# Kernel tuning notes

Measured on AMD Instinct MI355X. Metric: run time of the kernel, lower is better.

Reference implementation:

```python
import jax, jax.numpy as jnp
import numpy as np

N_NODES = 100000
N_EDGES = 500000
N_REL = 6
IN_DIM = 64
HID = 128
HEADS = 4
C = HID // HEADS  # 32 per-head channels
N_GRAPHS = 1024
EPS = 1e-16


def setup_inputs() -> dict:
    key = jax.random.key(0)
    ks = jax.random.split(key, 20)
    x = jax.random.normal(ks[0], (N_NODES, IN_DIM), dtype=jnp.float32)
    edge_index = jax.random.randint(ks[1], (N_REL, 2, N_EDGES), 0, N_NODES, dtype=jnp.int64)
    batch = jnp.sort(jax.random.randint(ks[2], (N_NODES,), 0, N_GRAPHS, dtype=jnp.int64))
    s = 0.02
    return {
        "x": x, "edge_index": edge_index, "batch": batch,
        # layer1 GAT params (stacked over 6 relations)
        "W1": jax.random.normal(ks[3], (N_REL, IN_DIM, HID), dtype=jnp.float32) * s,
        "as1": jax.random.normal(ks[4], (N_REL, HEADS, C), dtype=jnp.float32) * s,
        "ad1": jax.random.normal(ks[5], (N_REL, HEADS, C), dtype=jnp.float32) * s,
        "b1": jnp.zeros((N_REL, HID), dtype=jnp.float32),
        # layer2 GAT params
        "W2": jax.random.normal(ks[6], (N_REL, HID, HID), dtype=jnp.float32) * s,
        "as2": jax.random.normal(ks[7], (N_REL, HEADS, C), dtype=jnp.float32) * s,
        "ad2": jax.random.normal(ks[8], (N_REL, HEADS, C), dtype=jnp.float32) * s,
        "b2": jnp.zeros((N_REL, HID), dtype=jnp.float32),
        # layernorms
        "g1": jnp.ones((HID,), dtype=jnp.float32), "be1": jnp.zeros((HID,), dtype=jnp.float32),
        "g2": jnp.ones((HID,), dtype=jnp.float32), "be2": jnp.zeros((HID,), dtype=jnp.float32),
        # attention pooling query + output proj
        "q": jax.random.normal(ks[9], (HID,), dtype=jnp.float32) * s,
        "Wp": jax.random.normal(ks[10], (HID, HID), dtype=jnp.float32) * s,
        "bp": jnp.zeros((HID,), dtype=jnp.float32),
    }


def _gat_hetero_layer(x, edge_index, W, a_src, a_dst, b):
    # HeteroConv(aggr='sum') over R GATConv relations, add_self_loops=False, eval (no dropout)
    N = x.shape[0]
    out = jnp.zeros((N, HEADS * C), dtype=x.dtype)
    for r in range(N_REL):
        h = (x @ W[r]).reshape(N, HEADS, C)          # [N,H,C]
        al_s = (h * a_src[r]).sum(-1)                # [N,H]
        al_d = (h * a_dst[r]).sum(-1)                # [N,H]
        src, dst = edge_index[r, 0], edge_index[r, 1]
        e = jax.nn.leaky_relu(al_s[src] + al_d[dst], 0.2)   # [E,H]
        m = jax.ops.segment_max(e, dst, num_segments=N)
        ex = jnp.exp(e - m[dst])
        den = jax.ops.segment_sum(ex, dst, num_segments=N)
        alpha = ex / (den[dst] + EPS)                # segment softmax over incoming edges
        msg = h[src] * alpha[:, :, None]             # [E,H,C]
        agg = jax.ops.segment_sum(msg, dst, num_segments=N).reshape(N, HEADS * C)
        out = out + agg + b[r]
    return out


def _layernorm(x, g, b):
    mu = x.mean(-1, keepdims=True)
    v = ((x - mu) ** 2).mean(-1, keepdims=True)
    return (x - mu) * jax.lax.rsqrt(v + 1e-5) * g + b


def _softsign(x):
    return x / (1.0 + jnp.abs(x))


def reference(x, edge_index, batch, W1, as1, ad1, b1, W2, as2, ad2, b2,
              g1, be1, g2, be2, q, Wp, bp):
    h = _gat_hetero_layer(x, edge_index, W1, as1, ad1, b1)
    h = _layernorm(_softsign(h), g1, be1)
    h = _gat_hetero_layer(h, edge_index, W2, as2, ad2, b2)
    h = _layernorm(_softsign(h), g2, be2)
    # attention pooling: segment softmax over batch, then weighted scatter-sum
    scores = (h * q).sum(-1)                                   # [N]
    m = jax.ops.segment_max(scores, batch, num_segments=N_GRAPHS)
    ex = jnp.exp(scores - m[batch])
    den = jax.ops.segment_sum(ex, batch, num_segments=N_GRAPHS)
    w = ex / (den[batch] + EPS)
    pooled = jax.ops.segment_sum(h * w[:, None], batch, num_segments=N_GRAPHS)  # [G,HID]
    return pooled @ Wp + bp
```

## Files before the change

kernel.cpp:

```cpp
#include <hip/hip_runtime.h>
#include <hip/hip_bf16.h>
#include <hip/hip_fp16.h>

#define N_NODES_C 100000
#define N_EDGES_C 500000
#define N_REL_C 6
#define IN_DIM_C 64
#define HID_C 128
#define HEADS_C 4
#define CPH_C 32
#define N_GRAPHS_C 1024
#define NBLK_SCAN 391
#define SH_PAD 8

typedef _Float16 f16x8 __attribute__((ext_vector_type(8)));
typedef float f32x4 __attribute__((ext_vector_type(4)));

__global__ __launch_bounds__(256) void hist_rank_convert_kernel(
    const int* __restrict__ ei, int* __restrict__ cnt, int* __restrict__ rank,
    const float* __restrict__ x, __half* __restrict__ xh,
    const float* __restrict__ W1, const float* __restrict__ W2,
    __half* __restrict__ Wt1, __half* __restrict__ Wt2) {
    int i = blockIdx.x * 256 + threadIdx.x;
    if (i < N_NODES_C * IN_DIM_C / 4) {
        float4 v = ((const float4*)x)[i];
        union { __half h[4]; uint2 u; } u;
        u.h[0] = __float2half(v.x); u.h[1] = __float2half(v.y);
        u.h[2] = __float2half(v.z); u.h[3] = __float2half(v.w);
        ((uint2*)xh)[i] = u.u;
    }
    if (i < N_REL_C * IN_DIM_C * HID_C) {
        int r = i / (IN_DIM_C * HID_C);
        int rem = i - r * (IN_DIM_C * HID_C);
        int k = rem / HID_C, n = rem - k * HID_C;
        Wt1[(size_t)r * HID_C * IN_DIM_C + n * IN_DIM_C + k] = __float2half(W1[i]);
    }
    if (i < N_REL_C * HID_C * HID_C) {
        int r = i / (HID_C * HID_C);
        int rem = i - r * (HID_C * HID_C);
        int k = rem / HID_C, n = rem - k * HID_C;
        Wt2[(size_t)r * HID_C * HID_C + n * HID_C + k] = __float2half(W2[i]);
    }
    if (i < N_REL_C * N_EDGES_C) {
        int r = i / N_EDGES_C;
        int e = i - r * N_EDGES_C;
        int dst = ei[(size_t)r * 2 * N_EDGES_C + N_EDGES_C + e];
        rank[i] = atomicAdd(&cnt[r * N_NODES_C + dst], 1);
    }
}

__global__ __launch_bounds__(256) void scan1_kernel(const int* __restrict__ cnt,
                                                    int* __restrict__ rowptr,
                                                    int* __restrict__ blocksums) {
    int r = blockIdx.y, b = blockIdx.x, t = threadIdx.x;
    int idx = b * 256 + t;
    int v = (idx < N_NODES_C) ? cnt[r * N_NODES_C + idx] : 0;
    int orig = v;
    int lane = t & 63, w = t >> 6;
#pragma unroll
    for (int off = 1; off < 64; off <<= 1) {
        int n = __shfl_up(v, off);
        if (lane >= off) v += n;
    }
    __shared__ int wt[4];
    if (lane == 63) wt[w] = v;
    __syncthreads();
    int add = 0;
    for (int i = 0; i < w; i++) add += wt[i];
    v += add;
    if (idx < N_NODES_C) rowptr[(size_t)r * (N_NODES_C + 1) + idx] = v - orig;
    if (t == 255) blocksums[r * NBLK_SCAN + b] = v;
}

__global__ __launch_bounds__(512) void scan2_kernel(int* __restrict__ blocksums) {
    int r = blockIdx.x, t = threadIdx.x;
    int v = (t < NBLK_SCAN) ? blocksums[r * NBLK_SCAN + t] : 0;
    int orig = v;
    int lane = t & 63, w = t >> 6;
#pragma unroll
    for (int off = 1; off < 64; off <<= 1) {
        int n = __shfl_up(v, off);
        if (lane >= off) v += n;
    }
    __shared__ int wt[8];
    if (lane == 63) wt[w] = v;
    __syncthreads();
    int add = 0;
    for (int i = 0; i < w; i++) add += wt[i];
    v += add;
    if (t < NBLK_SCAN) blocksums[r * NBLK_SCAN + t] = v - orig;
}

__global__ __launch_bounds__(256) void scatter_kernel(const int* __restrict__ ei,
                                                      const int* __restrict__ rowptrP,
                                                      const int* __restrict__ bsums,
                                                      const int* __restrict__ rank,
                                                      int* __restrict__ srcids) {
    int i = blockIdx.x * 256 + threadIdx.x;
    if (i >= N_REL_C * N_EDGES_C) return;
    int r = i / N_EDGES_C;
    int e = i - r * N_EDGES_C;
    int src = ei[(size_t)r * 2 * N_EDGES_C + e];
    int dst = ei[(size_t)r * 2 * N_EDGES_C + N_EDGES_C + e];
    int base = rowptrP[(size_t)r * (N_NODES_C + 1) + dst] + bsums[r * NBLK_SCAN + (dst >> 8)];
    srcids[(size_t)r * N_EDGES_C + base + rank[i]] = src;
}

template <int K>
__global__ __launch_bounds__(256) void gemm_mfma_kernel(
    const __half* __restrict__ Xh, const __half* __restrict__ Wtbase,
    __half* __restrict__ Hbase,
    const float* __restrict__ asbase, const float* __restrict__ adbase,
    float* __restrict__ alsbase, float* __restrict__ aldbase) {
    __shared__ _Float16 sh[4][16][HID_C + SH_PAD];
    const int slot = blockIdx.y;
    const __half* Wt = Wtbase + (size_t)slot * HID_C * K;
    __half* H = Hbase + (size_t)slot * N_NODES_C * HID_C;
    const int wave = threadIdx.x >> 6, lane = threadIdx.x & 63;
    const int r0 = blockIdx.x * 64 + wave * 16;
    const int m = lane & 15, quad = lane >> 4;
    int arow = r0 + m;
    if (arow > N_NODES_C - 1) arow = N_NODES_C - 1;
    const __half* ap = Xh + (size_t)arow * K + quad * 8;
    const __half* bp = Wt + (size_t)m * K + quad * 8;

    f32x4 acc[8];
#pragma unroll
    for (int t = 0; t < 8; t++) acc[t] = (f32x4){0.f, 0.f, 0.f, 0.f};

#pragma unroll
    for (int kc = 0; kc < K; kc += 32) {
        f16x8 a = *(const f16x8*)(ap + kc);
#pragma unroll
        for (int t = 0; t < 8; t++) {
            f16x8 b = *(const f16x8*)(bp + (size_t)t * 16 * K + kc);
            acc[t] = __builtin_amdgcn_mfma_f32_16x16x32_f16(a, b, acc[t], 0, 0, 0);
        }
    }

#pragma unroll
    for (int t = 0; t < 8; t++)
#pragma unroll
        for (int i = 0; i < 4; i++)
            sh[wave][quad * 4 + i][t * 16 + m] = (_Float16)acc[t][i];
#pragma unroll
    for (int p = 0; p < 4; p++) {
        int idx = p * 512 + lane * 8;
        int row = idx >> 7;
        int col = idx & 127;
        int R = r0 + row;
        if (R < N_NODES_C)
            *(uint4*)(H + (size_t)R * HID_C + col) = *(const uint4*)&sh[wave][row][col];
    }

    const float* a_s = asbase + slot * HID_C;
    const float* a_d = adbase + slot * HID_C;
    float* als = alsbase + (size_t)slot * N_NODES_C * HEADS_C;
    float* ald = aldbase + (size_t)slot * N_NODES_C * HEADS_C;
    float ps[4][4], pd[4][4];
#pragma unroll
    for (int h = 0; h < 4; h++) {
        float as0 = a_s[h * 32 + m], as1 = a_s[h * 32 + 16 + m];
        float ad0 = a_d[h * 32 + m], ad1 = a_d[h * 32 + 16 + m];
#pragma unroll
        for (int i = 0; i < 4; i++) {
            ps[h][i] = acc[2 * h][i] * as0 + acc[2 * h + 1][i] * as1;
            pd[h][i] = acc[2 * h][i] * ad0 + acc[2 * h + 1][i] * ad1;
        }
    }
#pragma unroll
    for (int off = 1; off < 16; off <<= 1) {
#pragma unroll
        for (int h = 0; h < 4; h++)
#pragma unroll
            for (int i = 0; i < 4; i++) {
                ps[h][i] += __shfl_xor(ps[h][i], off);
                pd[h][i] += __shfl_xor(pd[h][i], off);
            }
    }
#pragma unroll
    for (int h = 0; h < 4; h++) {
        if (m == h) {
#pragma unroll
            for (int i = 0; i < 4; i++) {
                int R = r0 + quad * 4 + i;
                if (R < N_NODES_C) {
                    als[R * HEADS_C + h] = ps[h][i];
                    ald[R * HEADS_C + h] = pd[h][i];
                }
            }
        }
    }
}

__global__ __launch_bounds__(256) void csr_agg_kernel(
    const int* __restrict__ rowptrP, const int* __restrict__ bsums,
    const int* __restrict__ srcids,
    const __half* __restrict__ A, const float* __restrict__ als,
    const float* __restrict__ ald, int rel_start, int rel_cnt,
    const float* __restrict__ bias, int first, int last,
    float* __restrict__ B,
    const float* __restrict__ g, const float* __restrict__ be,
    __half* __restrict__ Cbh) {
    int node = blockIdx.x * 4 + (threadIdx.x >> 6);
    int lane = threadIdx.x & 63;
    int grp = lane >> 4;
    int j16 = lane & 15;
    int head = j16 >> 2;
    int cbase = j16 * 8;

    float acc[8];
    if (first) {
#pragma unroll
        for (int t = 0; t < 8; t++) {
            float s = 0.f;
#pragma unroll
            for (int r = 0; r < N_REL_C; r++) s += bias[r * HID_C + cbase + t];
            acc[t] = s;
        }
    } else {
        float4 b0 = *(const float4*)(B + (size_t)node * HID_C + cbase);
        float4 b1 = *(const float4*)(B + (size_t)node * HID_C + cbase + 4);
        acc[0] = b0.x; acc[1] = b0.y; acc[2] = b0.z; acc[3] = b0.w;
        acc[4] = b1.x; acc[5] = b1.y; acc[6] = b1.z; acc[7] = b1.w;
    }

    for (int j = 0; j < rel_cnt; j++) {
        int r = rel_start + j;
        const int* rp = rowptrP + (size_t)r * (N_NODES_C + 1);
        const int* bs = bsums + r * NBLK_SCAN;
        const int* sp = srcids + (size_t)r * N_EDGES_C;
        const __half* Aj = A + (size_t)j * N_NODES_C * HID_C;
        const float* alj = als + (size_t)j * N_NODES_C * HEADS_C;
        float aldv = ald[(size_t)j * N_NODES_C * HEADS_C + node * HEADS_C + head];
        int s = rp[node] + bs[node >> 8];
        int e = (node == N_NODES_C - 1) ? N_EDGES_C
                                        : rp[node + 1] + bs[(node + 1) >> 8];
        float racc[8];
#pragma unroll
        for (int t = 0; t < 8; t++) racc[t] = 0.f;
        float rden = 0.f;

        union HU { uint4 u; _Float16 h[8]; };
        int i = s + grp;
        int src = (i < e) ? sp[i] : 0;
        HU rw; rw.u = *(const uint4*)(Aj + (size_t)src * HID_C + cbase);
        float lg = alj[src * HEADS_C + head];
        for (; i < e; i += 4) {
            int nsrc = (i + 4 < e) ? sp[i + 4] : 0;
            HU nrw; nrw.u = *(const uint4*)(Aj + (size_t)nsrc * HID_C + cbase);
            float nlg = alj[nsrc * HEADS_C + head];
            float v = lg + aldv;
            v = fmaxf(v, 0.2f * v);
            float ex = __expf(v);
            rden += ex;
#pragma unroll
            for (int t = 0; t < 8; t++)
                racc[t] = fmaf((float)rw.h[t], ex, racc[t]);
            src = nsrc; rw = nrw; lg = nlg;
        }
#pragma unroll
        for (int off = 16; off < 64; off <<= 1) {
            rden += __shfl_xor(rden, off);
#pragma unroll
            for (int t = 0; t < 8; t++) racc[t] += __shfl_xor(racc[t], off);
        }
        float inv = 1.f / (rden + 1e-16f);
#pragma unroll
        for (int t = 0; t < 8; t++) acc[t] = fmaf(racc[t], inv, acc[t]);
    }

    if (!last) {
        if (grp == 0) {
            float4 o0 = make_float4(acc[0], acc[1], acc[2], acc[3]);
            float4 o1 = make_float4(acc[4], acc[5], acc[6], acc[7]);
            *(float4*)(B + (size_t)node * HID_C + cbase) = o0;
            *(float4*)(B + (size_t)node * HID_C + cbase + 4) = o1;
        }
    } else {
        float ss[8];
        float sum = 0.f, sq = 0.f;
#pragma unroll
        for (int t = 0; t < 8; t++) {
            float v = acc[t] / (1.f + fabsf(acc[t]));
            ss[t] = v;
            sum += v;
            sq = fmaf(v, v, sq);
        }
#pragma unroll
        for (int off = 1; off < 16; off <<= 1) {
            sum += __shfl_xor(sum, off);
            sq += __shfl_xor(sq, off);
        }
        float mu = sum * (1.f / 128.f);
        float var = sq * (1.f / 128.f) - mu * mu;
        float inv = rsqrtf(var + 1e-5f);
        if (grp == 0) {
            float4 gv0 = *(const float4*)(g + cbase);
            float4 gv1 = *(const float4*)(g + cbase + 4);
            float4 bv0 = *(const float4*)(be + cbase);
            float4 bv1 = *(const float4*)(be + cbase + 4);
            union { uint4 u; __half2 h2[4]; } ow;
            ow.h2[0] = __float22half2_rn(make_float2(
                (ss[0] - mu) * inv * gv0.x + bv0.x, (ss[1] - mu) * inv * gv0.y + bv0.y));
            ow.h2[1] = __float22half2_rn(make_float2(
                (ss[2] - mu) * inv * gv0.z + bv0.z, (ss[3] - mu) * inv * gv0.w + bv0.w));
            ow.h2[2] = __float22half2_rn(make_float2(
                (ss[4] - mu) * inv * gv1.x + bv1.x, (ss[5] - mu) * inv * gv1.y + bv1.y));
            ow.h2[3] = __float22half2_rn(make_float2(
                (ss[6] - mu) * inv * gv1.z + bv1.z, (ss[7] - mu) * inv * gv1.w + bv1.w));
            *(uint4*)(Cbh + (size_t)node * HID_C + cbase) = ow.u;
        }
    }
}

__device__ __forceinline__ int lower_bound_i(const int* __restrict__ a, int n, int v) {
    int lo = 0, hi = n;
    while (lo < hi) {
        int mid = (lo + hi) >> 1;
        if (a[mid] < v) lo = mid + 1; else hi = mid;
    }
    return lo;
}

__global__ __launch_bounds__(256) void pool_kernel(const __half* __restrict__ H,
                                                   const int* __restrict__ batch,
                                                   const float* __restrict__ q,
                                                   float* __restrict__ pooled) {
    int g = blockIdx.x;
    int t = threadIdx.x;
    int wave = t >> 6, lane = t & 63;
    int start = lower_bound_i(batch, N_NODES_C, g);
    int end = lower_bound_i(batch, N_NODES_C, g + 1);
    float q0 = q[lane * 2], q1 = q[lane * 2 + 1];
    float p0 = 0.f, p1 = 0.f, den = 0.f;
    for (int n = start + wave; n < end; n += 4) {
        float2 hv = __half22float2(*(const __half2*)(H + (size_t)n * HID_C + lane * 2));
        float part = hv.x * q0 + hv.y * q1;
#pragma unroll
        for (int off = 1; off < 64; off <<= 1) part += __shfl_xor(part, off);
        float exs = __expf(part);
        den += exs;
        p0 = fmaf(exs, hv.x, p0);
        p1 = fmaf(exs, hv.y, p1);
    }
    __shared__ float sp[4][HID_C];
    __shared__ float sden[4];
    sp[wave][lane * 2] = p0;
    sp[wave][lane * 2 + 1] = p1;
    if (lane == 0) sden[wave] = den;
    __syncthreads();
    if (wave == 0) {
        float a0 = sp[0][lane * 2] + sp[1][lane * 2] + sp[2][lane * 2] + sp[3][lane * 2];
        float a1 = sp[0][lane * 2 + 1] + sp[1][lane * 2 + 1] + sp[2][lane * 2 + 1] + sp[3][lane * 2 + 1];
        float d = sden[0] + sden[1] + sden[2] + sden[3];
        float w = 1.f / (d + 1e-16f);
        pooled[(size_t)g * HID_C + lane * 2] = a0 * w;
        pooled[(size_t)g * HID_C + lane * 2 + 1] = a1 * w;
    }
}

__global__ __launch_bounds__(128) void proj_kernel(const float* __restrict__ pooled,
                                                   const float* __restrict__ Wp,
                                                   const float* __restrict__ bp,
                                                   float* __restrict__ out) {
    int g = blockIdx.x, c = threadIdx.x;
    __shared__ float pl[HID_C];
    pl[c] = pooled[(size_t)g * HID_C + c];
    __syncthreads();
    float s = bp[c];
    for (int k = 0; k < HID_C; k++) s = fmaf(pl[k], Wp[k * HID_C + c], s);
    out[(size_t)g * HID_C + c] = s;
}

extern "C" void kernel_launch(void* const* d_in, const int* in_sizes, int n_in,
                              void* d_out, int out_size, void* d_ws, size_t ws_size,
                              hipStream_t stream) {
    const float* x   = (const float*)d_in[0];
    const int* ei    = (const int*)d_in[1];
    const int* batch = (const int*)d_in[2];
    const float* W1  = (const float*)d_in[3];
    const float* as1 = (const float*)d_in[4];
    const float* ad1 = (const float*)d_in[5];
    const float* b1  = (const float*)d_in[6];
    const float* W2  = (const float*)d_in[7];
    const float* as2 = (const float*)d_in[8];
    const float* ad2 = (const float*)d_in[9];
    const float* b2  = (const float*)d_in[10];
    const float* g1  = (const float*)d_in[11];
    const float* be1 = (const float*)d_in[12];
    const float* g2  = (const float*)d_in[13];
    const float* be2 = (const float*)d_in[14];
    const float* q   = (const float*)d_in[15];
    const float* Wp  = (const float*)d_in[16];
    const float* bp  = (const float*)d_in[17];
    float* out = (float*)d_out;

    const size_t NH = (size_t)N_NODES_C * HID_C;
    char* w = (char*)d_ws;
    __half* xh    = (__half*)w;   w += (size_t)N_NODES_C * IN_DIM_C * 2;
    __half* Cbh   = (__half*)w;   w += NH * 2;
    __half* Wt1   = (__half*)w;   w += (size_t)N_REL_C * IN_DIM_C * HID_C * 2;
    __half* Wt2   = (__half*)w;   w += (size_t)N_REL_C * HID_C * HID_C * 2;
    float* pooled = (float*)w;    w += (size_t)N_GRAPHS_C * HID_C * 4;
    int* rowptr   = (int*)w;      w += ((size_t)N_REL_C * (N_NODES_C + 1) * 4 + 15) & ~15ull;
    int* srcids   = (int*)w;      w += (size_t)N_REL_C * N_EDGES_C * 4;
    int* cnt      = (int*)w;      w += (size_t)N_REL_C * N_NODES_C * 4;
    int* bsums    = (int*)w;      w += ((size_t)N_REL_C * NBLK_SCAN * 4 + 15) & ~15ull;

    const size_t fixed_bytes = (size_t)(w - (char*)d_ws);
    const size_t slot_bytes = NH * 2 + 2 * (size_t)N_NODES_C * HEADS_C * 4;
    int nA = 1;
    float* B = nullptr;
    {
        size_t rem = (ws_size > fixed_bytes) ? (ws_size - fixed_bytes) : 0;
        size_t k = rem / slot_bytes;
        if (k >= 6) {
            nA = 6;
        } else {
            size_t rem2 = (rem > NH * 4) ? (rem - NH * 4) : 0;
            size_t k2 = rem2 / slot_bytes;
            nA = (int)(k2 < 1 ? 1 : (k2 > 5 ? 5 : k2));
        }
    }
    float* als = (float*)w;
    float* ald = als + (size_t)nA * N_NODES_C * HEADS_C;
    __half* A  = (__half*)(ald + (size_t)nA * N_NODES_C * HEADS_C);
    if (nA < 6) B = (float*)(A + (size_t)nA * NH);
    int* rank = (int*)A;

    hipMemsetAsync(cnt, 0, (size_t)N_REL_C * N_NODES_C * sizeof(int), stream);
    const int ehg = (N_REL_C * N_EDGES_C + 255) / 256;
    hist_rank_convert_kernel<<<ehg, 256, 0, stream>>>(ei, cnt, rank, x, xh, W1, W2, Wt1, Wt2);
    scan1_kernel<<<dim3(NBLK_SCAN, N_REL_C), 256, 0, stream>>>(cnt, rowptr, bsums);
    scan2_kernel<<<N_REL_C, 512, 0, stream>>>(bsums);
    scatter_kernel<<<ehg, 256, 0, stream>>>(ei, rowptr, bsums, rank, srcids);

    const int gemm_grid = (N_NODES_C + 63) / 64;
    const int agg_grid = N_NODES_C / 4;

    for (int gs = 0; gs < N_REL_C; gs += nA) {
        int c2 = (N_REL_C - gs) < nA ? (N_REL_C - gs) : nA;
        gemm_mfma_kernel<IN_DIM_C><<<dim3(gemm_grid, c2), 256, 0, stream>>>(
            xh, Wt1 + (size_t)gs * IN_DIM_C * HID_C, A,
            as1 + gs * HID_C, ad1 + gs * HID_C, als, ald);
        csr_agg_kernel<<<agg_grid, 256, 0, stream>>>(
            rowptr, bsums, srcids, A, als, ald, gs, c2,
            b1, (gs == 0) ? 1 : 0, (gs + c2 == N_REL_C) ? 1 : 0,
            B, g1, be1, Cbh);
    }
    for (int gs = 0; gs < N_REL_C; gs += nA) {
        int c2 = (N_REL_C - gs) < nA ? (N_REL_C - gs) : nA;
        gemm_mfma_kernel<HID_C><<<dim3(gemm_grid, c2), 256, 0, stream>>>(
            Cbh, Wt2 + (size_t)gs * HID_C * HID_C, A,
            as2 + gs * HID_C, ad2 + gs * HID_C, als, ald);
        csr_agg_kernel<<<agg_grid, 256, 0, stream>>>(
            rowptr, bsums, srcids, A, als, ald, gs, c2,
            b2, (gs == 0) ? 1 : 0, (gs + c2 == N_REL_C) ? 1 : 0,
            B, g2, be2, Cbh);
    }

    pool_kernel<<<N_GRAPHS_C, 256, 0, stream>>>(Cbh, batch, q, pooled);
    proj_kernel<<<N_GRAPHS_C, 128, 0, stream>>>(pooled, Wp, bp, out);
}
```

Baseline: 1.043 ms.

## Aggregate raw input features before projection in layer one GAT

Layer one no longer projects every node to 128 channels per relation before aggregating. The attention logits are computed directly from x using folded vectors W1·a. Then the 64-dim fp16 input features are aggregated per head along the CSR edges, and the aggregate is multiplied by W1 with MFMA in a fused kernel that also applies bias, softsign and layernorm. This cuts the 128-wide per-edge gathers down to 64-wide and removes the per-relation projected H buffers. In exchange it does four times the per-head accumulation in registers and rounds the aggregates to fp16 before the MFMA.

```diff
diff --git a/kernel.cpp b/kernel.cpp
--- a/kernel.cpp
+++ b/kernel.cpp
@@ -20,7 +20,9 @@
     const int* __restrict__ ei, int* __restrict__ cnt, int* __restrict__ rank,
     const float* __restrict__ x, __half* __restrict__ xh,
     const float* __restrict__ W1, const float* __restrict__ W2,
-    __half* __restrict__ Wt1, __half* __restrict__ Wt2) {
+    __half* __restrict__ Wt1, __half* __restrict__ Wt2,
+    const float* __restrict__ as1, const float* __restrict__ ad1,
+    float* __restrict__ wsd, float* __restrict__ wdd) {
     int i = blockIdx.x * 256 + threadIdx.x;
     if (i < N_NODES_C * IN_DIM_C / 4) {
         float4 v = ((const float4*)x)[i];
@@ -40,6 +42,19 @@
         int rem = i - r * (HID_C * HID_C);
         int k = rem / HID_C, n = rem - k * HID_C;
         Wt2[(size_t)r * HID_C * HID_C + n * HID_C + k] = __float2half(W2[i]);
+    }
+    if (i < N_REL_C * HEADS_C * IN_DIM_C) {
+        int r = i >> 8, h = (i >> 6) & 3, k = i & 63;
+        const float* wrow = W1 + ((size_t)(r * IN_DIM_C + k)) * HID_C + h * CPH_C;
+        const float* av_s = as1 + (r * HEADS_C + h) * CPH_C;
+        const float* av_d = ad1 + (r * HEADS_C + h) * CPH_C;
+        float ss = 0.f, sd = 0.f;
+#pragma unroll
+        for (int c = 0; c < CPH_C; c++) {
+            ss = fmaf(wrow[c], av_s[c], ss);
+            sd = fmaf(wrow[c], av_d[c], sd);
+        }
+        wsd[i] = ss; wdd[i] = sd;
     }
     if (i < N_REL_C * N_EDGES_C) {
         int r = i / N_EDGES_C;
@@ -104,6 +119,179 @@
     int dst = ei[(size_t)r * 2 * N_EDGES_C + N_EDGES_C + e];
     int base = rowptrP[(size_t)r * (N_NODES_C + 1) + dst] + bsums[r * NBLK_SCAN + (dst >> 8)];
     srcids[(size_t)r * N_EDGES_C + base + rank[i]] = src;
+}
+
+__global__ __launch_bounds__(256) void logit1_kernel(
+    const __half* __restrict__ xh, const float* __restrict__ wsd,
+    const float* __restrict__ wdd, float* __restrict__ als, float* __restrict__ ald) {
+    int wave = threadIdx.x >> 6, lane = threadIdx.x & 63;
+    int node = blockIdx.x * 4 + wave;
+    __shared__ float sx[4][IN_DIM_C];
+    if (lane < 32) {
+        float2 f = __half22float2(*(const __half2*)(xh + (size_t)node * IN_DIM_C + lane * 2));
+        sx[wave][lane * 2] = f.x;
+        sx[wave][lane * 2 + 1] = f.y;
+    }
+    __syncthreads();
+    if (lane < 48) {
+        int r = lane >> 3, rem = lane & 7;
+        int h = rem >> 1, sd = rem & 1;
+        const float* wp = (sd ? wdd : wsd) + (size_t)(r * HEADS_C + h) * IN_DIM_C;
+        float acc = 0.f;
+#pragma unroll
+        for (int k = 0; k < IN_DIM_C; k += 4) {
+            float4 wv = *(const float4*)(wp + k);
+            acc = fmaf(sx[wave][k], wv.x, acc);
+            acc = fmaf(sx[wave][k + 1], wv.y, acc);
+            acc = fmaf(sx[wave][k + 2], wv.z, acc);
+            acc = fmaf(sx[wave][k + 3], wv.w, acc);
+        }
+        float* dst = sd ? ald : als;
+        dst[((size_t)r * N_NODES_C + node) * HEADS_C + h] = acc;
+    }
+}
+
+__global__ __launch_bounds__(256) void agg1_kernel(
+    const int* __restrict__ rowptrP, const int* __restrict__ bsums,
+    const int* __restrict__ srcids, const __half* __restrict__ xh,
+    const float* __restrict__ als, const float* __restrict__ ald,
+    const __half* __restrict__ Wt1, const float* __restrict__ bias,
+    const float* __restrict__ g, const float* __restrict__ be,
+    __half* __restrict__ Cbh) {
+    __shared__ __align__(16) _Float16 S[HEADS_C][16][72];
+    __shared__ float sden[HEADS_C][16];
+    __shared__ float lnbuf[16][132];
+    const int wave = threadIdx.x >> 6, lane = threadIdx.x & 63;
+    const int grp = lane >> 4, j16 = lane & 15;
+    const int nbase = blockIdx.x * 16;
+    const int node = nbase + wave * 4 + grp;
+    const int nloc = wave * 4 + grp;
+
+    float facc[2][4] = {{0.f, 0.f, 0.f, 0.f}, {0.f, 0.f, 0.f, 0.f}};
+    float bsum[2];
+#pragma unroll
+    for (int nt = 0; nt < 2; nt++) {
+        int c = wave * 32 + nt * 16 + j16;
+        float sb = 0.f;
+#pragma unroll
+        for (int r = 0; r < N_REL_C; r++) sb += bias[r * HID_C + c];
+        bsum[nt] = sb;
+    }
+
+    for (int r = 0; r < N_REL_C; r++) {
+        const int* rp = rowptrP + (size_t)r * (N_NODES_C + 1);
+        const int* bs = bsums + r * NBLK_SCAN;
+        const int* sp = srcids + (size_t)r * N_EDGES_C;
+        const float* alr = als + (size_t)r * N_NODES_C * HEADS_C;
+        const float* adr = ald + (size_t)r * N_NODES_C * HEADS_C;
+
+        float adv[4];
+        {
+            float4 t = *(const float4*)(adr + (size_t)node * HEADS_C);
+            adv[0] = t.x; adv[1] = t.y; adv[2] = t.z; adv[3] = t.w;
+        }
+        int s = rp[node] + bs[node >> 8];
+        int e = (node == N_NODES_C - 1) ? N_EDGES_C : rp[node + 1] + bs[(node + 1) >> 8];
+
+        float racc[4][4];
+#pragma unroll
+        for (int h = 0; h < 4; h++)
+#pragma unroll
+            for (int j = 0; j < 4; j++) racc[h][j] = 0.f;
+        float rden[4] = {0.f, 0.f, 0.f, 0.f};
+
+        int i = s;
+        int src = (i < e) ? sp[i] : 0;
+        uint2 xw = *(const uint2*)(xh + (size_t)src * IN_DIM_C + j16 * 4);
+        float4 lg = *(const float4*)(alr + (size_t)src * HEADS_C);
+        for (; i < e; i++) {
+            int nsrc = (i + 1 < e) ? sp[i + 1] : 0;
+            uint2 nxw = *(const uint2*)(xh + (size_t)nsrc * IN_DIM_C + j16 * 4);
+            float4 nlg = *(const float4*)(alr + (size_t)nsrc * HEADS_C);
+            float ex0, ex1, ex2, ex3;
+            {
+                float v0 = lg.x + adv[0]; v0 = fmaxf(v0, 0.2f * v0); ex0 = __expf(v0);
+                float v1 = lg.y + adv[1]; v1 = fmaxf(v1, 0.2f * v1); ex1 = __expf(v1);
+                float v2 = lg.z + adv[2]; v2 = fmaxf(v2, 0.2f * v2); ex2 = __expf(v2);
+                float v3 = lg.w + adv[3]; v3 = fmaxf(v3, 0.2f * v3); ex3 = __expf(v3);
+            }
+            rden[0] += ex0; rden[1] += ex1; rden[2] += ex2; rden[3] += ex3;
+            union { uint2 u; _Float16 hh[4]; } xu;
+            xu.u = xw;
+            float xf0 = (float)xu.hh[0], xf1 = (float)xu.hh[1];
+            float xf2 = (float)xu.hh[2], xf3 = (float)xu.hh[3];
+            racc[0][0] = fmaf(xf0, ex0, racc[0][0]); racc[0][1] = fmaf(xf1, ex0, racc[0][1]);
+            racc[0][2] = fmaf(xf2, ex0, racc[0][2]); racc[0][3] = fmaf(xf3, ex0, racc[0][3]);
+            racc[1][0] = fmaf(xf0, ex1, racc[1][0]); racc[1][1] = fmaf(xf1, ex1, racc[1][1]);
+            racc[1][2] = fmaf(xf2, ex1, racc[1][2]); racc[1][3] = fmaf(xf3, ex1, racc[1][3]);
+            racc[2][0] = fmaf(xf0, ex2, racc[2][0]); racc[2][1] = fmaf(xf1, ex2, racc[2][1]);
+            racc[2][2] = fmaf(xf2, ex2, racc[2][2]); racc[2][3] = fmaf(xf3, ex2, racc[2][3]);
+            racc[3][0] = fmaf(xf0, ex3, racc[3][0]); racc[3][1] = fmaf(xf1, ex3, racc[3][1]);
+            racc[3][2] = fmaf(xf2, ex3, racc[3][2]); racc[3][3] = fmaf(xf3, ex3, racc[3][3]);
+            src = nsrc; xw = nxw; lg = nlg;
+        }
+
+#pragma unroll
+        for (int h = 0; h < 4; h++) {
+            __half2 p0 = __float22half2_rn(make_float2(racc[h][0], racc[h][1]));
+            __half2 p1 = __float22half2_rn(make_float2(racc[h][2], racc[h][3]));
+            *(__half2*)&S[h][nloc][j16 * 4] = p0;
+            *(__half2*)&S[h][nloc][j16 * 4 + 2] = p1;
+        }
+        if (j16 == 0) {
+#pragma unroll
+            for (int h = 0; h < 4; h++) sden[h][nloc] = 1.f / (rden[h] + 1e-16f);
+        }
+        __syncthreads();
+
+        const __half* Wr = Wt1 + (size_t)r * HID_C * IN_DIM_C;
+        f32x4 acc0 = {0.f, 0.f, 0.f, 0.f}, acc1 = {0.f, 0.f, 0.f, 0.f};
+#pragma unroll
+        for (int kc = 0; kc < 2; kc++) {
+            f16x8 a = *(const f16x8*)&S[wave][j16][kc * 32 + grp * 8];
+            f16x8 b0 = *(const f16x8*)(Wr + (size_t)(wave * 32 + j16) * IN_DIM_C + kc * 32 + grp * 8);
+            f16x8 b1 = *(const f16x8*)(Wr + (size_t)(wave * 32 + 16 + j16) * IN_DIM_C + kc * 32 + grp * 8);
+            acc0 = __builtin_amdgcn_mfma_f32_16x16x32_f16(a, b0, acc0, 0, 0, 0);
+            acc1 = __builtin_amdgcn_mfma_f32_16x16x32_f16(a, b1, acc1, 0, 0, 0);
+        }
+#pragma unroll
+        for (int ii = 0; ii < 4; ii++) {
+            float inv = sden[wave][grp * 4 + ii];
+            facc[0][ii] = fmaf(acc0[ii], inv, facc[0][ii]);
+            facc[1][ii] = fmaf(acc1[ii], inv, facc[1][ii]);
+        }
+        __syncthreads();
+    }
+
+#pragma unroll
+    for (int nt = 0; nt < 2; nt++)
+#pragma unroll
+        for (int ii = 0; ii < 4; ii++) {
+            float v = facc[nt][ii] + bsum[nt];
+            v = v / (1.f + fabsf(v));
+            lnbuf[grp * 4 + ii][wave * 32 + nt * 16 + j16] = v;
+        }
+    __syncthreads();
+#pragma unroll
+    for (int jj = 0; jj < 4; jj++) {
+        int nl = wave * 4 + jj;
+        float2 v = *(const float2*)&lnbuf[nl][lane * 2];
+        float sum = v.x + v.y;
+        float sq = v.x * v.x + v.y * v.y;
+#pragma unroll
+        for (int off = 1; off < 64; off <<= 1) {
+            sum += __shfl_xor(sum, off);
+            sq += __shfl_xor(sq, off);
+        }
+        float mu = sum * (1.f / 128.f);
+        float var = sq * (1.f / 128.f) - mu * mu;
+        float inv = rsqrtf(var + 1e-5f);
+        float2 gv = *(const float2*)(g + lane * 2);
+        float2 bv = *(const float2*)(be + lane * 2);
+        __half2 o = __float22half2_rn(make_float2((v.x - mu) * inv * gv.x + bv.x,
+                                                  (v.y - mu) * inv * gv.y + bv.y));
+        *(__half2*)(Cbh + (size_t)(nbase + nl) * HID_C + lane * 2) = o;
+    }
 }
 
 template <int K>
@@ -427,28 +615,27 @@
     float* ald = als + (size_t)nA * N_NODES_C * HEADS_C;
     __half* A  = (__half*)(ald + (size_t)nA * N_NODES_C * HEADS_C);
     if (nA < 6) B = (float*)(A + (size_t)nA * NH);
+
     int* rank = (int*)A;
+    float* wsd1 = pooled;
+    float* wdd1 = pooled + (size_t)N_REL_C * HEADS_C * IN_DIM_C;
+    float* als1 = (float*)A;
+    float* ald1 = als1 + (size_t)N_REL_C * N_NODES_C * HEADS_C;
 
     hipMemsetAsync(cnt, 0, (size_t)N_REL_C * N_NODES_C * sizeof(int), stream);
     const int ehg = (N_REL_C * N_EDGES_C + 255) / 256;
-    hist_rank_convert_kernel<<<ehg, 256, 0, stream>>>(ei, cnt, rank, x, xh, W1, W2, Wt1, Wt2);
+    hist_rank_convert_kernel<<<ehg, 256, 0, stream>>>(ei, cnt, rank, x, xh, W1, W2,
+                                                      Wt1, Wt2, as1, ad1, wsd1, wdd1);
     scan1_kernel<<<dim3(NBLK_SCAN, N_REL_C), 256, 0, stream>>>(cnt, rowptr, bsums);
     scan2_kernel<<<N_REL_C, 512, 0, stream>>>(bsums);
     scatter_kernel<<<ehg, 256, 0, stream>>>(ei, rowptr, bsums, rank, srcids);
 
+    logit1_kernel<<<N_NODES_C / 4, 256, 0, stream>>>(xh, wsd1, wdd1, als1, ald1);
+    agg1_kernel<<<N_NODES_C / 16, 256, 0, stream>>>(rowptr, bsums, srcids, xh,
+                                                    als1, ald1, Wt1, b1, g1, be1, Cbh);
+
     const int gemm_grid = (N_NODES_C + 63) / 64;
     const int agg_grid = N_NODES_C / 4;
-
-    for (int gs = 0; gs < N_REL_C; gs += nA) {
-        int c2 = (N_REL_C - gs) < nA ? (N_REL_C - gs) : nA;
-        gemm_mfma_kernel<IN_DIM_C><<<dim3(gemm_grid, c2), 256, 0, stream>>>(
-            xh, Wt1 + (size_t)gs * IN_DIM_C * HID_C, A,
-            as1 + gs * HID_C, ad1 + gs * HID_C, als, ald);
-        csr_agg_kernel<<<agg_grid, 256, 0, stream>>>(
-            rowptr, bsums, srcids, A, als, ald, gs, c2,
-            b1, (gs == 0) ? 1 : 0, (gs + c2 == N_REL_C) ? 1 : 0,
-            B, g1, be1, Cbh);
-    }
     for (int gs = 0; gs < N_REL_C; gs += nA) {
         int c2 = (N_REL_C - gs) < nA ? (N_REL_C - gs) : nA;
         gemm_mfma_kernel<HID_C><<<dim3(gemm_grid, c2), 256, 0, stream>>>(
```

New measurement: 1.203 ms. +15.4%, slower.
